# Kernel tuning notes

Hardware: AMD Instinct MI355X
Metric: run time of the kernel (lower is better)

## Reference

```python
import jax, jax.numpy as jnp
import numpy as np

B_, T, I, S, O = 64, 2048, 64, 128, 64

def setup_inputs() -> dict:
    key = jax.random.key(0)
    ks = jax.random.split(key, 7)
    x = jax.random.normal(ks[0], (B_, T, I), dtype=jnp.float32)
    A = jax.random.normal(ks[1], (S, S), dtype=jnp.float32) * 0.1
    Bm = jax.random.normal(ks[2], (S, I), dtype=jnp.float32) * 0.1
    Cm = jax.random.normal(ks[3], (O, S), dtype=jnp.float32) * 0.1
    Dm = jax.random.normal(ks[4], (O, I), dtype=jnp.float32) * 0.1
    W_sel = jax.random.normal(ks[5], (S, I), dtype=jnp.float32) * 0.1
    b_sel = jnp.zeros((S,), jnp.float32)
    ln_gamma = jnp.ones((S,), jnp.float32)
    ln_beta = jnp.zeros((S,), jnp.float32)
    conv_w = jax.random.normal(ks[6], (S, I, 3), dtype=jnp.float32) * 0.1  # Conv1d weight [out,in,k]
    conv_b = jnp.zeros((S,), jnp.float32)
    return {"x": x, "A": A, "B": Bm, "C": Cm, "D": Dm, "W_sel": W_sel,
            "b_sel": b_sel, "ln_gamma": ln_gamma, "ln_beta": ln_beta,
            "conv_w": conv_w, "conv_b": conv_b, "use_parallel": 0}

LN_EPS = 1e-5

def _forward(x, A, B, C, D, W_sel, b_sel, ln_gamma, ln_beta, conv_w, conv_b, use_parallel):
    # x: [B, T, I]
    if use_parallel and x.shape[1] > 10:
        # parallel_scan: conv1d(k=3, pad=1) -> cumsum over time -> project with C
        xc = jnp.transpose(x, (0, 2, 1))  # [B, I, T]
        conv = jax.lax.conv_general_dilated(
            xc, conv_w, window_strides=(1,), padding=((1, 1),),
            dimension_numbers=("NCH", "OIH", "NCH")) + conv_b[None, :, None]
        conv = jnp.transpose(conv, (0, 2, 1))           # [B, T, S]
        out = jnp.cumsum(conv, axis=1) @ C.T            # [B, T, O]
    else:
        # selective_scan: sequential gated SSM with per-step LayerNorm
        def step(h, x_t):
            gate = jax.nn.sigmoid(x_t @ W_sel.T + b_sel)        # [B, S]
            h_new = h @ A.T + x_t @ B.T
            h = gate * h_new + (1.0 - gate) * h
            mu = jnp.mean(h, axis=-1, keepdims=True)
            var = jnp.var(h, axis=-1, keepdims=True)
            h = (h - mu) * jax.lax.rsqrt(var + LN_EPS) * ln_gamma + ln_beta
            y = h @ C.T + x_t @ D.T                              # [B, O]
            return h, y
        h0 = jnp.zeros((x.shape[0], A.shape[0]), x.dtype)
        _, ys = jax.lax.scan(step, h0, jnp.transpose(x, (1, 0, 2)))  # ys: [T, B, O]
        out = jnp.transpose(ys, (1, 0, 2))                           # [B, T, O]
    final = out[:, -1, :]
    diff = jnp.diff(out, axis=1)
    temporal_coherence = 1.0 / (1.0 + jnp.mean(jnp.linalg.norm(diff, axis=-1)))
    state_magnitude = jnp.mean(jnp.linalg.norm(out, axis=-1))
    selection_activity = jnp.mean(jax.nn.sigmoid(jnp.mean(x, axis=1) @ W_sel.T + b_sel))
    state_stability = jnp.mean(jnp.std(out, axis=1, ddof=1))  # torch.std is unbiased
    return final, temporal_coherence, state_magnitude, selection_activity, state_stability

def reference(x, A, B, C, D, W_sel, b_sel, ln_gamma, ln_beta, conv_w, conv_b, use_parallel):
    return _forward(x, A, B, C, D, W_sel, b_sel, ln_gamma, ln_beta, conv_w, conv_b, use_parallel)
```

## Files before the change

### kernel.cpp

```cpp
#include <hip/hip_runtime.h>
#include <math.h>

#define NB 64
#define NT 2048
#define NI 64
#define NS 128
#define NO 64

typedef float4 f4;

#define PIN4(v) asm("" : "+v"((v).x), "+v"((v).y), "+v"((v).z), "+v"((v).w))

#define FMA4(a0,a1,a2,a3,W_,V_) \
    a0 = fmaf((W_).x, (V_).x, a0); a1 = fmaf((W_).y, (V_).y, a1); \
    a2 = fmaf((W_).z, (V_).z, a2); a3 = fmaf((W_).w, (V_).w, a3)

template<int CTRL>
__device__ __forceinline__ float dpp_add(float v) {
    int t = __builtin_amdgcn_update_dpp(0, __float_as_int(v), CTRL, 0xF, 0xF, true);
    return v + __int_as_float(t);
}
__device__ __forceinline__ float qxor1(float v) { return dpp_add<0xB1>(v); }
__device__ __forceinline__ float qxor2(float v) { return dpp_add<0x4E>(v); }
__device__ __forceinline__ float wave_sum63(float v) {
    v = dpp_add<0x111>(v); v = dpp_add<0x112>(v); v = dpp_add<0x114>(v);
    v = dpp_add<0x118>(v); v = dpp_add<0x142>(v); v = dpp_add<0x143>(v);
    return v;
}

__device__ __forceinline__ float sigmoidf_fast(float z) {
    float e = __builtin_amdgcn_exp2f(z * -1.442695041f);
    return __builtin_amdgcn_rcpf(1.0f + e);
}

__device__ __forceinline__ void bar_lds() {
    asm volatile("s_waitcnt lgkmcnt(0)" ::: "memory");
    __builtin_amdgcn_s_barrier();
    asm volatile("" ::: "memory");
}

__device__ __forceinline__ void stage16(const float* g, float* l) {
    __builtin_amdgcn_global_load_lds(
        (const __attribute__((address_space(1))) void*)g,
        (__attribute__((address_space(3))) void*)l, 16, 0, 0);
}

__global__ __launch_bounds__(512, 2) void scan_kernel(
    const float* __restrict__ x,
    const float* __restrict__ A,
    const float* __restrict__ Bm,
    const float* __restrict__ Wsel,
    const float* __restrict__ bsel,
    const float* __restrict__ gamma,
    const float* __restrict__ beta,
    float* __restrict__ H,
    float* __restrict__ musig)
{
    const int b    = blockIdx.x;
    const int tid  = threadIdx.x;
    const int q    = tid & 3;
    const int r    = tid >> 2;
    const int lane = tid & 63;
    const int wave = tid >> 6;

    __shared__ __align__(16) float hbuf[2][148];
    __shared__ __align__(16) float red[2][16];
    __shared__ __align__(16) float xlds[2][32][64];

    f4 Aw0, Aw1, Aw2, Aw3, Aw4, Aw5, Aw6, Aw7;
    float sAg = 0.f, aB = 0.f;
    {
        const f4* ga = (const f4*)(gamma + q * 32);
        const f4* bb = (const f4*)(beta  + q * 32);
        const f4* Ap = (const f4*)(A + (size_t)r * NS + q * 32);
        f4 g, be_, v;
#define LOADA(J, AW) \
        g = ga[J]; be_ = bb[J]; v = Ap[J]; \
        AW.x = v.x * g.x; AW.y = v.y * g.y; AW.z = v.z * g.z; AW.w = v.w * g.w; \
        sAg += (AW.x + AW.y) + (AW.z + AW.w); \
        aB = fmaf(v.x, be_.x, aB); aB = fmaf(v.y, be_.y, aB); \
        aB = fmaf(v.z, be_.z, aB); aB = fmaf(v.w, be_.w, aB);
        LOADA(0, Aw0) LOADA(1, Aw1) LOADA(2, Aw2) LOADA(3, Aw3)
        LOADA(4, Aw4) LOADA(5, Aw5) LOADA(6, Aw6) LOADA(7, Aw7)
#undef LOADA
        sAg = qxor2(qxor1(sAg));
        aB  = qxor2(qxor1(aB));
    }
    f4 Bw0, Bw1, Bw2, Bw3, Ww0, Ww1, Ww2, Ww3;
    {
        const f4* Bp = (const f4*)(Bm   + (size_t)r * NI + q * 16);
        const f4* Wp = (const f4*)(Wsel + (size_t)r * NI + q * 16);
        Bw0 = Bp[0]; Bw1 = Bp[1]; Bw2 = Bp[2]; Bw3 = Bp[3];
        Ww0 = Wp[0]; Ww1 = Wp[1]; Ww2 = Wp[2]; Ww3 = Wp[3];
    }
    float bs = bsel[r], gm = gamma[r], bt = beta[r];

    PIN4(Aw0); PIN4(Aw1); PIN4(Aw2); PIN4(Aw3);
    PIN4(Aw4); PIN4(Aw5); PIN4(Aw6); PIN4(Aw7);
    PIN4(Bw0); PIN4(Bw1); PIN4(Bw2); PIN4(Bw3);
    PIN4(Ww0); PIN4(Ww1); PIN4(Ww2); PIN4(Ww3);
    asm("" : "+v"(sAg), "+v"(aB), "+v"(bs), "+v"(gm), "+v"(bt));

    const float* xstage = x + (size_t)b * NT * NI + wave * 256 + lane * 4;
    stage16(xstage,        &xlds[0][wave * 4][0]);
    stage16(xstage + 2048, &xlds[1][wave * 4][0]);
    asm volatile("s_waitcnt vmcnt(0)" ::: "memory");
    __syncthreads();

    float zp, dBp;
    auto xdots = [&](int t) {
        const f4* xp = (const f4*)&xlds[(t >> 5) & 1][t & 31][q * 16];
        f4 v0 = xp[0], v1 = xp[1], v2 = xp[2], v3 = xp[3];
        float p0 = 0.f, p1 = 0.f, p2 = 0.f, p3 = 0.f;
        float w0 = 0.f, w1 = 0.f, w2 = 0.f, w3 = 0.f;
        FMA4(p0, p1, p2, p3, Bw0, v0); FMA4(p0, p1, p2, p3, Bw1, v1);
        FMA4(p0, p1, p2, p3, Bw2, v2); FMA4(p0, p1, p2, p3, Bw3, v3);
        FMA4(w0, w1, w2, w3, Ww0, v0); FMA4(w0, w1, w2, w3, Ww1, v1);
        FMA4(w0, w1, w2, w3, Ww2, v2); FMA4(w0, w1, w2, w3, Ww3, v3);
        dBp = qxor2(qxor1((p0 + p1) + (p2 + p3)));
        zp  = qxor2(qxor1((w0 + w1) + (w2 + w3))) + bs;
    };

    float*  Hb   = H + ((size_t)b * NT) * NS;
    float2* musb = (float2*)musig + (size_t)b * NT;

    float mp;
    xdots(0);
    {
        float g = sigmoidf_fast(zp);
        mp = g * dBp;
        if (q == 0) {
            hbuf[0][((r >> 5) * 36) + (r & 31)] = mp;
            Hb[r] = mp;
        }
        float s  = wave_sum63(mp);
        float s2 = wave_sum63(mp * mp);
        if (lane == 63) { red[0][wave] = s; red[0][8 + wave] = s2; }
    }
    xdots(1);
    bar_lds();

    auto body = [&](int t, int parIn, int parOut) {
        const f4* rp = (const f4*)&red[parIn][0];
        f4 sa = rp[0], sb = rp[1], sc = rp[2], sd = rp[3];
        float S  = ((sa.x + sa.y) + (sa.z + sa.w)) + ((sb.x + sb.y) + (sb.z + sb.w));
        float S2 = ((sc.x + sc.y) + (sc.z + sc.w)) + ((sd.x + sd.y) + (sd.z + sd.w));
        float mu   = S * (1.0f / 512.0f);
        float var  = fmaf(S2, 1.0f / 512.0f, -mu * mu);
        float rstd = 1.0f / sqrtf(var + 1e-5f);
        const f4* hp = (const f4*)&hbuf[parIn][q * 36];
        f4 h0 = hp[0], h1 = hp[1], h2 = hp[2], h3 = hp[3];
        f4 h4 = hp[4], h5 = hp[5], h6 = hp[6], h7 = hp[7];
        float d0 = 0.f, d1 = 0.f, d2 = 0.f, d3 = 0.f;
        FMA4(d0, d1, d2, d3, Aw0, h0); FMA4(d0, d1, d2, d3, Aw1, h1);
        FMA4(d0, d1, d2, d3, Aw2, h2); FMA4(d0, d1, d2, d3, Aw3, h3);
        FMA4(d0, d1, d2, d3, Aw4, h4); FMA4(d0, d1, d2, d3, Aw5, h5);
        FMA4(d0, d1, d2, d3, Aw6, h6); FMA4(d0, d1, d2, d3, Aw7, h7);
        float dAm = qxor2(qxor1((d0 + d1) + (d2 + d3)));
        float dA  = fmaf(rstd, fmaf(-mu, sAg, dAm), aB);
        float hpl = fmaf((mp - mu) * rstd, gm, bt);
        float g  = sigmoidf_fast(zp);
        float hn = dA + dBp;
        float m  = fmaf(g, hn - hpl, hpl);
        if (q == 0) {
            hbuf[parOut][((r >> 5) * 36) + (r & 31)] = m;
            Hb[(size_t)t * NS + r] = m;
        }
        float s  = wave_sum63(m);
        float s2 = wave_sum63(m * m);
        if (lane == 63) { red[parOut][wave] = s; red[parOut][8 + wave] = s2; }
        if (tid == 0) musb[t - 1] = make_float2(mu, rstd);
        mp = m;
        if (t + 1 < NT) xdots(t + 1);
        bar_lds();
    };

    auto boundary = [&](int t) {
        const int s2 = (t >> 5) + 2;
        if (s2 < NT / 32)
            stage16(xstage + (size_t)s2 * 2048, &xlds[s2 & 1][wave * 4][0]);
        asm volatile("s_waitcnt vmcnt(1)" ::: "memory");
        __builtin_amdgcn_s_barrier();
        asm volatile("" ::: "memory");
    };

    for (int t = 1; t + 1 < NT; t += 2) {
        body(t, 0, 1);
        body(t + 1, 1, 0);
        if (((t + 1) & 31) == 30) boundary(t + 1);
    }
    body(NT - 1, 0, 1);

    {
        const f4* rp = (const f4*)&red[1][0];
        f4 sa = rp[0], sb = rp[1], sc = rp[2], sd = rp[3];
        float S  = ((sa.x + sa.y) + (sa.z + sa.w)) + ((sb.x + sb.y) + (sb.z + sb.w));
        float S2 = ((sc.x + sc.y) + (sc.z + sc.w)) + ((sd.x + sd.y) + (sd.z + sd.w));
        float mu   = S * (1.0f / 512.0f);
        float var  = fmaf(S2, 1.0f / 512.0f, -mu * mu);
        float rstd = 1.0f / sqrtf(var + 1e-5f);
        if (tid == 0) musb[NT - 1] = make_float2(mu, rstd);
    }
}

#define CHUNKS 32
#define TCH (NT / CHUNKS)

__global__ __launch_bounds__(512, 2) void y_stats_kernel(
    const float* __restrict__ H,
    const float* __restrict__ x,
    const float* __restrict__ Cm,
    const float* __restrict__ Dm,
    const float* __restrict__ gamma,
    const float* __restrict__ beta,
    const float* __restrict__ musig,
    float* __restrict__ SY,
    float* __restrict__ SYY,
    float* __restrict__ meanx,
    float* __restrict__ nsum,
    float* __restrict__ dsum,
    float* __restrict__ outFinal)
{
    const int b     = blockIdx.x >> 5;
    const int chunk = blockIdx.x & 31;
    const int tid   = threadIdx.x;
    const int o     = tid & 63;
    const int sub   = tid >> 6;
    const int kh    = sub & 1;
    const int tg    = sub >> 1;
    const int lane  = tid & 63;

    __shared__ float pbuf[TCH + 1][2 * NO];
    __shared__ float nd[2];

    f4 C0,C1,C2,C3,C4,C5,C6,C7,C8,C9,C10,C11,C12,C13,C14,C15;
    float sCg = 0.f, cB = 0.f;
    {
        const f4* cp = (const f4*)(Cm + (size_t)o * NS + kh * 64);
        const f4* gp = (const f4*)(gamma + kh * 64);
        const f4* bp = (const f4*)(beta  + kh * 64);
        f4 v, g, be;
#define LOADC(J, CW) \
        v = cp[J]; g = gp[J]; be = bp[J]; \
        CW.x = v.x * g.x; CW.y = v.y * g.y; CW.z = v.z * g.z; CW.w = v.w * g.w; \
        sCg += (CW.x + CW.y) + (CW.z + CW.w); \
        cB = fmaf(v.x, be.x, cB); cB = fmaf(v.y, be.y, cB); \
        cB = fmaf(v.z, be.z, cB); cB = fmaf(v.w, be.w, cB);
        LOADC(0,C0) LOADC(1,C1) LOADC(2,C2) LOADC(3,C3)
        LOADC(4,C4) LOADC(5,C5) LOADC(6,C6) LOADC(7,C7)
        LOADC(8,C8) LOADC(9,C9) LOADC(10,C10) LOADC(11,C11)
        LOADC(12,C12) LOADC(13,C13) LOADC(14,C14) LOADC(15,C15)
#undef LOADC
    }
    f4 D0,D1,D2,D3,D4,D5,D6,D7;
    {
        const f4* dp = (const f4*)(Dm + (size_t)o * NI + kh * 32);
        D0 = dp[0]; D1 = dp[1]; D2 = dp[2]; D3 = dp[3];
        D4 = dp[4]; D5 = dp[5]; D6 = dp[6]; D7 = dp[7];
    }
    PIN4(C0); PIN4(C1); PIN4(C2); PIN4(C3); PIN4(C4); PIN4(C5); PIN4(C6); PIN4(C7);
    PIN4(C8); PIN4(C9); PIN4(C10); PIN4(C11); PIN4(C12); PIN4(C13); PIN4(C14); PIN4(C15);
    PIN4(D0); PIN4(D1); PIN4(D2); PIN4(D3); PIN4(D4); PIN4(D5); PIN4(D6); PIN4(D7);
    asm("" : "+v"(sCg), "+v"(cB));

    const float*  Hb  = H + ((size_t)b * NT) * NS;
    const float*  xb  = x + ((size_t)b * NT) * NI;
    const float2* msb = (const float2*)musig + (size_t)b * NT;
    const int t0 = chunk * TCH;

    if (tid < 2) nd[tid] = 0.f;

    if (sub < 4) {
        float s = 0.f;
        const float* xk = xb + o;
        #pragma unroll 4
        for (int i = 0; i < 16; ++i) s += xk[(size_t)(t0 + sub * 16 + i) * NI];
        atomicAdd(&meanx[b * NI + o], s);
    }

    {
        const int i_start = (tg == 0 && t0 > 0) ? -1 : 0;
        for (int i = i_start; i < 16; ++i) {
            const int t = t0 + tg * 16 + i;
            float2 ms = msb[t];
            const f4* hp = (const f4*)(Hb + (size_t)t * NS + kh * 64);
            const f4* xp = (const f4*)(xb + (size_t)t * NI + kh * 32);
            float y0 = 0.f, y1 = 0.f, y2 = 0.f, y3 = 0.f;
            f4 hv;
            hv = hp[0];  FMA4(y0,y1,y2,y3,C0,hv);
            hv = hp[1];  FMA4(y0,y1,y2,y3,C1,hv);
            hv = hp[2];  FMA4(y0,y1,y2,y3,C2,hv);
            hv = hp[3];  FMA4(y0,y1,y2,y3,C3,hv);
            hv = hp[4];  FMA4(y0,y1,y2,y3,C4,hv);
            hv = hp[5];  FMA4(y0,y1,y2,y3,C5,hv);
            hv = hp[6];  FMA4(y0,y1,y2,y3,C6,hv);
            hv = hp[7];  FMA4(y0,y1,y2,y3,C7,hv);
            hv = hp[8];  FMA4(y0,y1,y2,y3,C8,hv);
            hv = hp[9];  FMA4(y0,y1,y2,y3,C9,hv);
            hv = hp[10]; FMA4(y0,y1,y2,y3,C10,hv);
            hv = hp[11]; FMA4(y0,y1,y2,y3,C11,hv);
            hv = hp[12]; FMA4(y0,y1,y2,y3,C12,hv);
            hv = hp[13]; FMA4(y0,y1,y2,y3,C13,hv);
            hv = hp[14]; FMA4(y0,y1,y2,y3,C14,hv);
            hv = hp[15]; FMA4(y0,y1,y2,y3,C15,hv);
            float hdot = (y0 + y1) + (y2 + y3);
            float x0 = 0.f, x1 = 0.f, x2 = 0.f, x3 = 0.f;
            hv = xp[0];  FMA4(x0,x1,x2,x3,D0,hv);
            hv = xp[1];  FMA4(x0,x1,x2,x3,D1,hv);
            hv = xp[2];  FMA4(x0,x1,x2,x3,D2,hv);
            hv = xp[3];  FMA4(x0,x1,x2,x3,D3,hv);
            hv = xp[4];  FMA4(x0,x1,x2,x3,D4,hv);
            hv = xp[5];  FMA4(x0,x1,x2,x3,D5,hv);
            hv = xp[6];  FMA4(x0,x1,x2,x3,D6,hv);
            hv = xp[7];  FMA4(x0,x1,x2,x3,D7,hv);
            float xdot = (x0 + x1) + (x2 + x3);
            pbuf[tg * 16 + i + 1][kh * 64 + o] =
                fmaf(ms.y, fmaf(-ms.x, sCg, hdot), cB + xdot);
        }
    }
    __syncthreads();

    {
        const int tt0 = sub * 8;
        float yprev = pbuf[tt0][o] + pbuf[tt0][64 + o];
        float sy = 0.f, syy = 0.f, na = 0.f, da = 0.f;
        #pragma unroll
        for (int ii = 0; ii < 8; ++ii) {
            const int row = tt0 + ii + 1;
            float y = pbuf[row][o] + pbuf[row][64 + o];
            sy  += y;
            syy += y * y;
            float n2 = wave_sum63(y * y);
            na += sqrtf(n2);
            if (t0 + tt0 + ii > 0) {
                float df = y - yprev;
                float d2 = wave_sum63(df * df);
                da += sqrtf(d2);
            }
            yprev = y;
            if (chunk == 31 && sub == 7 && ii == 7)
                outFinal[b * NO + o] = y;
        }
        atomicAdd(&SY[b * NO + o], sy);
        atomicAdd(&SYY[b * NO + o], syy);
        if (lane == 63) {
            atomicAdd(&nd[0], na);
            atomicAdd(&nd[1], da);
        }
    }
    __syncthreads();
    if (tid == 0) { atomicAdd(nsum, nd[0]); atomicAdd(dsum, nd[1]); }
}

__global__ __launch_bounds__(256) void finalize_kernel(
    const float* __restrict__ Wsel,
    const float* __restrict__ bsel,
    const float* __restrict__ meanx,
    const float* __restrict__ SY,
    const float* __restrict__ SYY,
    const float* __restrict__ nsum,
    const float* __restrict__ dsum,
    float* __restrict__ out)
{
    const int tid  = threadIdx.x;
    const int wave = tid >> 6;
    const int lane = tid & 63;
    __shared__ float rs[8];

    float accsel = 0.f;
    for (int idx = tid; idx < NB * NS; idx += 256) {
        int bb = idx >> 7;
        int s  = idx & 127;
        const float* mp = meanx + bb * NI;
        const float* wp = Wsel  + (size_t)s * NI;
        float dot = 0.f;
        #pragma unroll 8
        for (int k = 0; k < NI; ++k) dot = fmaf(mp[k], wp[k], dot);
        float z = fmaf(dot, 1.0f / NT, bsel[s]);
        accsel += 1.0f / (1.0f + expf(-z));
    }
    float accss = 0.f;
    for (int idx = tid; idx < NB * NO; idx += 256) {
        float s1 = SY[idx], s2 = SYY[idx];
        float var = (s2 - s1 * s1 * (1.0f / NT)) * (1.0f / (NT - 1));
        accss += sqrtf(fmaxf(var, 0.0f));
    }
    #pragma unroll
    for (int d = 1; d < 64; d <<= 1) {
        accsel += __shfl_xor(accsel, d);
        accss  += __shfl_xor(accss, d);
    }
    if (lane == 0) { rs[wave] = accsel; rs[4 + wave] = accss; }
    __syncthreads();
    if (tid == 0) {
        float sel = (rs[0] + rs[1] + rs[2] + rs[3]) / (float)(NB * NS);
        float ss  = (rs[4] + rs[5] + rs[6] + rs[7]) / (float)(NB * NO);
        float tc  = 1.0f / (1.0f + dsum[0] / (float)(NB * (NT - 1)));
        float sm  = nsum[0] / (float)(NB * NT);
        out[4096] = tc;
        out[4097] = sm;
        out[4098] = sel;
        out[4099] = ss;
    }
}

extern "C" void kernel_launch(void* const* d_in, const int* in_sizes, int n_in,
                              void* d_out, int out_size, void* d_ws, size_t ws_size,
                              hipStream_t stream)
{
    (void)in_sizes; (void)n_in; (void)out_size; (void)ws_size;
    const float* x     = (const float*)d_in[0];
    const float* A     = (const float*)d_in[1];
    const float* Bm    = (const float*)d_in[2];
    const float* Cm    = (const float*)d_in[3];
    const float* Dm    = (const float*)d_in[4];
    const float* Wsel  = (const float*)d_in[5];
    const float* bsel  = (const float*)d_in[6];
    const float* gamma = (const float*)d_in[7];
    const float* beta  = (const float*)d_in[8];
    float* out = (float*)d_out;

    char* ws = (char*)d_ws;
    size_t off = 0;
    float* H     = (float*)(ws + off); off += (size_t)NB * NT * NS * sizeof(float);
    float* musig = (float*)(ws + off); off += (size_t)NB * NT * 2 * sizeof(float);
    char*  zbase = ws + off;
    float* SY    = (float*)(ws + off); off += NB * NO * sizeof(float);
    float* SYY   = (float*)(ws + off); off += NB * NO * sizeof(float);
    float* meanx = (float*)(ws + off); off += NB * NI * sizeof(float);
    float* nsum  = (float*)(ws + off); off += sizeof(float);
    float* dsum  = (float*)(ws + off); off += sizeof(float);
    size_t zbytes = (size_t)((char*)(dsum + 1) - zbase);

    hipMemsetAsync(zbase, 0, zbytes, stream);
    scan_kernel<<<NB, 512, 0, stream>>>(x, A, Bm, Wsel, bsel, gamma, beta, H, musig);
    y_stats_kernel<<<NB * CHUNKS, 512, 0, stream>>>(H, x, Cm, Dm, gamma, beta, musig,
                                                    SY, SYY, meanx, nsum, dsum, out);
    finalize_kernel<<<1, 256, 0, stream>>>(Wsel, bsel, meanx, SY, SYY, nsum, dsum, out);
}
```

Measured before the change: 1.943 ms.

## Precompute input projections in a parallel kernel before the sequential scan

Adds a parallel projection kernel that computes x·Bᵀ and x·W_selᵀ+b for all timesteps into a workspace buffer. The sequential scan then only reads the precomputed values from LDS, which takes those dot products and their cross-lane reductions off the serial critical path. The y_stats kernel is also reworked so each thread computes two output columns over a quarter of the state, combined with a lane shuffle. The cost is an extra 128 MB write/read of the projection buffer, a larger LDS staging footprint in the scan, and a fallback path when the workspace is too small.

```diff
diff --git a/kernel.cpp b/kernel.cpp
--- a/kernel.cpp
+++ b/kernel.cpp
@@ -10,7 +10,6 @@
 typedef float4 f4;
 
 #define PIN4(v) asm("" : "+v"((v).x), "+v"((v).y), "+v"((v).z), "+v"((v).w))
-
 #define FMA4(a0,a1,a2,a3,W_,V_) \
     a0 = fmaf((W_).x, (V_).x, a0); a1 = fmaf((W_).y, (V_).y, a1); \
     a2 = fmaf((W_).z, (V_).z, a2); a3 = fmaf((W_).w, (V_).w, a3)
@@ -27,26 +26,84 @@
     v = dpp_add<0x118>(v); v = dpp_add<0x142>(v); v = dpp_add<0x143>(v);
     return v;
 }
-
 __device__ __forceinline__ float sigmoidf_fast(float z) {
     float e = __builtin_amdgcn_exp2f(z * -1.442695041f);
     return __builtin_amdgcn_rcpf(1.0f + e);
 }
-
 __device__ __forceinline__ void bar_lds() {
     asm volatile("s_waitcnt lgkmcnt(0)" ::: "memory");
     __builtin_amdgcn_s_barrier();
     asm volatile("" ::: "memory");
 }
-
 __device__ __forceinline__ void stage16(const float* g, float* l) {
     __builtin_amdgcn_global_load_lds(
         (const __attribute__((address_space(1))) void*)g,
         (__attribute__((address_space(3))) void*)l, 16, 0, 0);
 }
 
+__global__ __launch_bounds__(256, 2) void proj_kernel(
+    const float* __restrict__ x,
+    const float* __restrict__ Bm,
+    const float* __restrict__ Wsel,
+    const float* __restrict__ bsel,
+    float* __restrict__ P)
+{
+    const int b   = blockIdx.x >> 5;
+    const int c   = blockIdx.x & 31;
+    const int tid = threadIdx.x;
+
+    __shared__ __align__(16) float xs[64][64];
+    {
+        const f4* src = (const f4*)(x + ((size_t)b * NT + c * 64) * NI);
+        f4* dst = (f4*)&xs[0][0];
+        #pragma unroll
+        for (int k = 0; k < 4; ++k) dst[tid + k * 256] = src[tid + k * 256];
+    }
+
+    const float* wrow = (tid < 128) ? (Bm + (size_t)tid * NI)
+                                    : (Wsel + (size_t)(tid - 128) * NI);
+    const float bias = (tid < 128) ? 0.f : bsel[tid - 128];
+
+    f4 W0,W1,W2,W3,W4,W5,W6,W7,W8,W9,W10,W11,W12,W13,W14,W15;
+    {
+        const f4* wp = (const f4*)wrow;
+        W0=wp[0]; W1=wp[1]; W2=wp[2]; W3=wp[3]; W4=wp[4]; W5=wp[5]; W6=wp[6]; W7=wp[7];
+        W8=wp[8]; W9=wp[9]; W10=wp[10]; W11=wp[11]; W12=wp[12]; W13=wp[13]; W14=wp[14]; W15=wp[15];
+    }
+    PIN4(W0); PIN4(W1); PIN4(W2); PIN4(W3); PIN4(W4); PIN4(W5); PIN4(W6); PIN4(W7);
+    PIN4(W8); PIN4(W9); PIN4(W10); PIN4(W11); PIN4(W12); PIN4(W13); PIN4(W14); PIN4(W15);
+
+    __syncthreads();
+
+    float* pout = P + ((size_t)b * NT + c * 64) * 256 + tid;
+    for (int t = 0; t < 64; ++t) {
+        const f4* xr = (const f4*)&xs[t][0];
+        float a0 = bias, a1 = 0.f, a2 = 0.f, a3 = 0.f;
+        f4 v;
+        v = xr[0];  FMA4(a0,a1,a2,a3,W0,v);
+        v = xr[1];  FMA4(a0,a1,a2,a3,W1,v);
+        v = xr[2];  FMA4(a0,a1,a2,a3,W2,v);
+        v = xr[3];  FMA4(a0,a1,a2,a3,W3,v);
+        v = xr[4];  FMA4(a0,a1,a2,a3,W4,v);
+        v = xr[5];  FMA4(a0,a1,a2,a3,W5,v);
+        v = xr[6];  FMA4(a0,a1,a2,a3,W6,v);
+        v = xr[7];  FMA4(a0,a1,a2,a3,W7,v);
+        v = xr[8];  FMA4(a0,a1,a2,a3,W8,v);
+        v = xr[9];  FMA4(a0,a1,a2,a3,W9,v);
+        v = xr[10]; FMA4(a0,a1,a2,a3,W10,v);
+        v = xr[11]; FMA4(a0,a1,a2,a3,W11,v);
+        v = xr[12]; FMA4(a0,a1,a2,a3,W12,v);
+        v = xr[13]; FMA4(a0,a1,a2,a3,W13,v);
+        v = xr[14]; FMA4(a0,a1,a2,a3,W14,v);
+        v = xr[15]; FMA4(a0,a1,a2,a3,W15,v);
+        pout[(size_t)t * 256] = (a0 + a1) + (a2 + a3);
+    }
+}
+
+template<int USEP>
 __global__ __launch_bounds__(512, 2) void scan_kernel(
     const float* __restrict__ x,
+    const float* __restrict__ P,
     const float* __restrict__ A,
     const float* __restrict__ Bm,
     const float* __restrict__ Wsel,
@@ -65,7 +122,7 @@
 
     __shared__ __align__(16) float hbuf[2][148];
     __shared__ __align__(16) float red[2][16];
-    __shared__ __align__(16) float xlds[2][32][64];
+    __shared__ __align__(16) float plds[2][32][USEP ? 256 : 64];
 
     f4 Aw0, Aw1, Aw2, Aw3, Aw4, Aw5, Aw6, Aw7;
     float sAg = 0.f, aB = 0.f;
@@ -86,30 +143,44 @@
         sAg = qxor2(qxor1(sAg));
         aB  = qxor2(qxor1(aB));
     }
+    PIN4(Aw0); PIN4(Aw1); PIN4(Aw2); PIN4(Aw3);
+    PIN4(Aw4); PIN4(Aw5); PIN4(Aw6); PIN4(Aw7);
+
     f4 Bw0, Bw1, Bw2, Bw3, Ww0, Ww1, Ww2, Ww3;
-    {
+    float bs = 0.f;
+    if constexpr (!USEP) {
         const f4* Bp = (const f4*)(Bm   + (size_t)r * NI + q * 16);
         const f4* Wp = (const f4*)(Wsel + (size_t)r * NI + q * 16);
         Bw0 = Bp[0]; Bw1 = Bp[1]; Bw2 = Bp[2]; Bw3 = Bp[3];
         Ww0 = Wp[0]; Ww1 = Wp[1]; Ww2 = Wp[2]; Ww3 = Wp[3];
-    }
-    float bs = bsel[r], gm = gamma[r], bt = beta[r];
-
-    PIN4(Aw0); PIN4(Aw1); PIN4(Aw2); PIN4(Aw3);
-    PIN4(Aw4); PIN4(Aw5); PIN4(Aw6); PIN4(Aw7);
-    PIN4(Bw0); PIN4(Bw1); PIN4(Bw2); PIN4(Bw3);
-    PIN4(Ww0); PIN4(Ww1); PIN4(Ww2); PIN4(Ww3);
-    asm("" : "+v"(sAg), "+v"(aB), "+v"(bs), "+v"(gm), "+v"(bt));
+        bs = bsel[r];
+        PIN4(Bw0); PIN4(Bw1); PIN4(Bw2); PIN4(Bw3);
+        PIN4(Ww0); PIN4(Ww1); PIN4(Ww2); PIN4(Ww3);
+        asm("" : "+v"(bs));
+    }
+    float gm = gamma[r], bt = beta[r];
+    asm("" : "+v"(sAg), "+v"(aB), "+v"(gm), "+v"(bt));
 
     const float* xstage = x + (size_t)b * NT * NI + wave * 256 + lane * 4;
-    stage16(xstage,        &xlds[0][wave * 4][0]);
-    stage16(xstage + 2048, &xlds[1][wave * 4][0]);
+    const float* pstage = P + (size_t)b * NT * 256 + wave * 256 + lane * 4;
+    if constexpr (USEP) {
+        #pragma unroll
+        for (int c = 0; c < 2; ++c)
+            #pragma unroll
+            for (int k = 0; k < 4; ++k)
+                stage16(pstage + (size_t)(c * 32 + k * 8) * 256,
+                        &plds[c][k * 8 + wave][0]);
+    } else {
+        stage16(xstage,        &plds[0][wave * 4][0]);
+        stage16(xstage + 2048, &plds[1][wave * 4][0]);
+    }
     asm volatile("s_waitcnt vmcnt(0)" ::: "memory");
     __syncthreads();
 
-    float zp, dBp;
+    float zp = 0.f, dBp = 0.f;
+    float pbp = 0.f, pzp = 0.f;
     auto xdots = [&](int t) {
-        const f4* xp = (const f4*)&xlds[(t >> 5) & 1][t & 31][q * 16];
+        const f4* xp = (const f4*)&plds[(t >> 5) & 1][t & 31][q * 16];
         f4 v0 = xp[0], v1 = xp[1], v2 = xp[2], v3 = xp[3];
         float p0 = 0.f, p1 = 0.f, p2 = 0.f, p3 = 0.f;
         float w0 = 0.f, w1 = 0.f, w2 = 0.f, w3 = 0.f;
@@ -120,15 +191,19 @@
         dBp = qxor2(qxor1((p0 + p1) + (p2 + p3)));
         zp  = qxor2(qxor1((w0 + w1) + (w2 + w3))) + bs;
     };
+    auto pread = [&](int t) {
+        const float* pl = &plds[(t >> 5) & 1][t & 31][0];
+        pbp = pl[r]; pzp = pl[128 + r];
+    };
 
     float*  Hb   = H + ((size_t)b * NT) * NS;
     float2* musb = (float2*)musig + (size_t)b * NT;
 
     float mp;
-    xdots(0);
-    {
-        float g = sigmoidf_fast(zp);
-        mp = g * dBp;
+    if constexpr (USEP) pread(0); else xdots(0);
+    {
+        float g = sigmoidf_fast(USEP ? pzp : zp);
+        mp = g * (USEP ? pbp : dBp);
         if (q == 0) {
             hbuf[0][((r >> 5) * 36) + (r & 31)] = mp;
             Hb[r] = mp;
@@ -137,7 +212,7 @@
         float s2 = wave_sum63(mp * mp);
         if (lane == 63) { red[0][wave] = s; red[0][8 + wave] = s2; }
     }
-    xdots(1);
+    if constexpr (USEP) pread(1); else xdots(1);
     bar_lds();
 
     auto body = [&](int t, int parIn, int parOut) {
@@ -159,9 +234,9 @@
         float dAm = qxor2(qxor1((d0 + d1) + (d2 + d3)));
         float dA  = fmaf(rstd, fmaf(-mu, sAg, dAm), aB);
         float hpl = fmaf((mp - mu) * rstd, gm, bt);
-        float g  = sigmoidf_fast(zp);
-        float hn = dA + dBp;
-        float m  = fmaf(g, hn - hpl, hpl);
+        float g   = sigmoidf_fast(USEP ? pzp : zp);
+        float hn  = dA + (USEP ? pbp : dBp);
+        float m   = fmaf(g, hn - hpl, hpl);
         if (q == 0) {
             hbuf[parOut][((r >> 5) * 36) + (r & 31)] = m;
             Hb[(size_t)t * NS + r] = m;
@@ -171,15 +246,25 @@
         if (lane == 63) { red[parOut][wave] = s; red[parOut][8 + wave] = s2; }
         if (tid == 0) musb[t - 1] = make_float2(mu, rstd);
         mp = m;
-        if (t + 1 < NT) xdots(t + 1);
+        if (t + 1 < NT) { if constexpr (USEP) pread(t + 1); else xdots(t + 1); }
         bar_lds();
     };
 
     auto boundary = [&](int t) {
         const int s2 = (t >> 5) + 2;
-        if (s2 < NT / 32)
-            stage16(xstage + (size_t)s2 * 2048, &xlds[s2 & 1][wave * 4][0]);
-        asm volatile("s_waitcnt vmcnt(1)" ::: "memory");
+        if constexpr (USEP) {
+            if (s2 < NT / 32) {
+                #pragma unroll
+                for (int k = 0; k < 4; ++k)
+                    stage16(pstage + (size_t)(s2 * 32 + k * 8) * 256,
+                            &plds[s2 & 1][k * 8 + wave][0]);
+            }
+            asm volatile("s_waitcnt vmcnt(4)" ::: "memory");
+        } else {
+            if (s2 < NT / 32)
+                stage16(xstage + (size_t)s2 * 2048, &plds[s2 & 1][wave * 4][0]);
+            asm volatile("s_waitcnt vmcnt(1)" ::: "memory");
+        }
         __builtin_amdgcn_s_barrier();
         asm volatile("" ::: "memory");
     };
@@ -206,7 +291,7 @@
 #define CHUNKS 32
 #define TCH (NT / CHUNKS)
 
-__global__ __launch_bounds__(512, 2) void y_stats_kernel(
+__global__ __launch_bounds__(512, 1) void y_stats_kernel(
     const float* __restrict__ H,
     const float* __restrict__ x,
     const float* __restrict__ Cm,
@@ -224,44 +309,47 @@
     const int b     = blockIdx.x >> 5;
     const int chunk = blockIdx.x & 31;
     const int tid   = threadIdx.x;
+    const int o2    = tid & 31;
+    const int kq    = (tid >> 5) & 3;
+    const int tg    = tid >> 7;
+    const int lane  = tid & 63;
+    const int sub   = tid >> 6;
     const int o     = tid & 63;
-    const int sub   = tid >> 6;
-    const int kh    = sub & 1;
-    const int tg    = sub >> 1;
-    const int lane  = tid & 63;
 
     __shared__ float pbuf[TCH + 1][2 * NO];
     __shared__ float nd[2];
 
-    f4 C0,C1,C2,C3,C4,C5,C6,C7,C8,C9,C10,C11,C12,C13,C14,C15;
-    float sCg = 0.f, cB = 0.f;
-    {
-        const f4* cp = (const f4*)(Cm + (size_t)o * NS + kh * 64);
-        const f4* gp = (const f4*)(gamma + kh * 64);
-        const f4* bp = (const f4*)(beta  + kh * 64);
-        f4 v, g, be;
-#define LOADC(J, CW) \
-        v = cp[J]; g = gp[J]; be = bp[J]; \
-        CW.x = v.x * g.x; CW.y = v.y * g.y; CW.z = v.z * g.z; CW.w = v.w * g.w; \
-        sCg += (CW.x + CW.y) + (CW.z + CW.w); \
-        cB = fmaf(v.x, be.x, cB); cB = fmaf(v.y, be.y, cB); \
-        cB = fmaf(v.z, be.z, cB); cB = fmaf(v.w, be.w, cB);
-        LOADC(0,C0) LOADC(1,C1) LOADC(2,C2) LOADC(3,C3)
-        LOADC(4,C4) LOADC(5,C5) LOADC(6,C6) LOADC(7,C7)
-        LOADC(8,C8) LOADC(9,C9) LOADC(10,C10) LOADC(11,C11)
-        LOADC(12,C12) LOADC(13,C13) LOADC(14,C14) LOADC(15,C15)
-#undef LOADC
-    }
-    f4 D0,D1,D2,D3,D4,D5,D6,D7;
-    {
-        const f4* dp = (const f4*)(Dm + (size_t)o * NI + kh * 32);
-        D0 = dp[0]; D1 = dp[1]; D2 = dp[2]; D3 = dp[3];
-        D4 = dp[4]; D5 = dp[5]; D6 = dp[6]; D7 = dp[7];
-    }
-    PIN4(C0); PIN4(C1); PIN4(C2); PIN4(C3); PIN4(C4); PIN4(C5); PIN4(C6); PIN4(C7);
-    PIN4(C8); PIN4(C9); PIN4(C10); PIN4(C11); PIN4(C12); PIN4(C13); PIN4(C14); PIN4(C15);
-    PIN4(D0); PIN4(D1); PIN4(D2); PIN4(D3); PIN4(D4); PIN4(D5); PIN4(D6); PIN4(D7);
-    asm("" : "+v"(sCg), "+v"(cB));
+    f4 CA0,CA1,CA2,CA3,CA4,CA5,CA6,CA7, CB0,CB1,CB2,CB3,CB4,CB5,CB6,CB7;
+    float sCgA = 0.f, cBA = 0.f, sCgB = 0.f, cBB = 0.f;
+    {
+        const f4* cpA = (const f4*)(Cm + (size_t)o2 * NS + kq * 32);
+        const f4* cpB = (const f4*)(Cm + (size_t)(o2 + 32) * NS + kq * 32);
+        const f4* gp  = (const f4*)(gamma + kq * 32);
+        const f4* bp  = (const f4*)(beta  + kq * 32);
+        f4 vv, gg, bb;
+#define LC(J, CW, CP, SG, CBs) \
+        vv = CP[J]; gg = gp[J]; bb = bp[J]; \
+        CW.x = vv.x * gg.x; CW.y = vv.y * gg.y; CW.z = vv.z * gg.z; CW.w = vv.w * gg.w; \
+        SG += (CW.x + CW.y) + (CW.z + CW.w); \
+        CBs = fmaf(vv.x, bb.x, CBs); CBs = fmaf(vv.y, bb.y, CBs); \
+        CBs = fmaf(vv.z, bb.z, CBs); CBs = fmaf(vv.w, bb.w, CBs);
+        LC(0,CA0,cpA,sCgA,cBA) LC(1,CA1,cpA,sCgA,cBA) LC(2,CA2,cpA,sCgA,cBA) LC(3,CA3,cpA,sCgA,cBA)
+        LC(4,CA4,cpA,sCgA,cBA) LC(5,CA5,cpA,sCgA,cBA) LC(6,CA6,cpA,sCgA,cBA) LC(7,CA7,cpA,sCgA,cBA)
+        LC(0,CB0,cpB,sCgB,cBB) LC(1,CB1,cpB,sCgB,cBB) LC(2,CB2,cpB,sCgB,cBB) LC(3,CB3,cpB,sCgB,cBB)
+        LC(4,CB4,cpB,sCgB,cBB) LC(5,CB5,cpB,sCgB,cBB) LC(6,CB6,cpB,sCgB,cBB) LC(7,CB7,cpB,sCgB,cBB)
+#undef LC
+    }
+    f4 DA0,DA1,DA2,DA3, DB0,DB1,DB2,DB3;
+    {
+        const f4* dpA = (const f4*)(Dm + (size_t)o2 * NI + kq * 16);
+        const f4* dpB = (const f4*)(Dm + (size_t)(o2 + 32) * NI + kq * 16);
+        DA0 = dpA[0]; DA1 = dpA[1]; DA2 = dpA[2]; DA3 = dpA[3];
+        DB0 = dpB[0]; DB1 = dpB[1]; DB2 = dpB[2]; DB3 = dpB[3];
+    }
+    PIN4(CA0); PIN4(CA1); PIN4(CA2); PIN4(CA3); PIN4(CA4); PIN4(CA5); PIN4(CA6); PIN4(CA7);
+    PIN4(CB0); PIN4(CB1); PIN4(CB2); PIN4(CB3); PIN4(CB4); PIN4(CB5); PIN4(CB6); PIN4(CB7);
+    PIN4(DA0); PIN4(DA1); PIN4(DA2); PIN4(DA3); PIN4(DB0); PIN4(DB1); PIN4(DB2); PIN4(DB3);
+    asm("" : "+v"(sCgA), "+v"(cBA), "+v"(sCgB), "+v"(cBB));
 
     const float*  Hb  = H + ((size_t)b * NT) * NS;
     const float*  xb  = x + ((size_t)b * NT) * NI;
@@ -279,43 +367,39 @@
     }
 
     {
+        const int khigh = sub & 1;
         const int i_start = (tg == 0 && t0 > 0) ? -1 : 0;
         for (int i = i_start; i < 16; ++i) {
             const int t = t0 + tg * 16 + i;
             float2 ms = msb[t];
-            const f4* hp = (const f4*)(Hb + (size_t)t * NS + kh * 64);
-            const f4* xp = (const f4*)(xb + (size_t)t * NI + kh * 32);
-            float y0 = 0.f, y1 = 0.f, y2 = 0.f, y3 = 0.f;
+            const f4* hp = (const f4*)(Hb + (size_t)t * NS + kq * 32);
+            const f4* xp = (const f4*)(xb + (size_t)t * NI + kq * 16);
+            float a0=0.f,a1=0.f,a2=0.f,a3=0.f, b0=0.f,b1=0.f,b2=0.f,b3=0.f;
             f4 hv;
-            hv = hp[0];  FMA4(y0,y1,y2,y3,C0,hv);
-            hv = hp[1];  FMA4(y0,y1,y2,y3,C1,hv);
-            hv = hp[2];  FMA4(y0,y1,y2,y3,C2,hv);
-            hv = hp[3];  FMA4(y0,y1,y2,y3,C3,hv);
-            hv = hp[4];  FMA4(y0,y1,y2,y3,C4,hv);
-            hv = hp[5];  FMA4(y0,y1,y2,y3,C5,hv);
-            hv = hp[6];  FMA4(y0,y1,y2,y3,C6,hv);
-            hv = hp[7];  FMA4(y0,y1,y2,y3,C7,hv);
-            hv = hp[8];  FMA4(y0,y1,y2,y3,C8,hv);
-            hv = hp[9];  FMA4(y0,y1,y2,y3,C9,hv);
-            hv = hp[10]; FMA4(y0,y1,y2,y3,C10,hv);
-            hv = hp[11]; FMA4(y0,y1,y2,y3,C11,hv);
-            hv = hp[12]; FMA4(y0,y1,y2,y3,C12,hv);
-            hv = hp[13]; FMA4(y0,y1,y2,y3,C13,hv);
-            hv = hp[14]; FMA4(y0,y1,y2,y3,C14,hv);
-            hv = hp[15]; FMA4(y0,y1,y2,y3,C15,hv);
-            float hdot = (y0 + y1) + (y2 + y3);
-            float x0 = 0.f, x1 = 0.f, x2 = 0.f, x3 = 0.f;
-            hv = xp[0];  FMA4(x0,x1,x2,x3,D0,hv);
-            hv = xp[1];  FMA4(x0,x1,x2,x3,D1,hv);
-            hv = xp[2];  FMA4(x0,x1,x2,x3,D2,hv);
-            hv = xp[3];  FMA4(x0,x1,x2,x3,D3,hv);
-            hv = xp[4];  FMA4(x0,x1,x2,x3,D4,hv);
-            hv = xp[5];  FMA4(x0,x1,x2,x3,D5,hv);
-            hv = xp[6];  FMA4(x0,x1,x2,x3,D6,hv);
-            hv = xp[7];  FMA4(x0,x1,x2,x3,D7,hv);
-            float xdot = (x0 + x1) + (x2 + x3);
-            pbuf[tg * 16 + i + 1][kh * 64 + o] =
-                fmaf(ms.y, fmaf(-ms.x, sCg, hdot), cB + xdot);
+            hv = hp[0]; FMA4(a0,a1,a2,a3,CA0,hv); FMA4(b0,b1,b2,b3,CB0,hv);
+            hv = hp[1]; FMA4(a0,a1,a2,a3,CA1,hv); FMA4(b0,b1,b2,b3,CB1,hv);
+            hv = hp[2]; FMA4(a0,a1,a2,a3,CA2,hv); FMA4(b0,b1,b2,b3,CB2,hv);
+            hv = hp[3]; FMA4(a0,a1,a2,a3,CA3,hv); FMA4(b0,b1,b2,b3,CB3,hv);
+            hv = hp[4]; FMA4(a0,a1,a2,a3,CA4,hv); FMA4(b0,b1,b2,b3,CB4,hv);
+            hv = hp[5]; FMA4(a0,a1,a2,a3,CA5,hv); FMA4(b0,b1,b2,b3,CB5,hv);
+            hv = hp[6]; FMA4(a0,a1,a2,a3,CA6,hv); FMA4(b0,b1,b2,b3,CB6,hv);
+            hv = hp[7]; FMA4(a0,a1,a2,a3,CA7,hv); FMA4(b0,b1,b2,b3,CB7,hv);
+            float hdotA = (a0 + a1) + (a2 + a3);
+            float hdotB = (b0 + b1) + (b2 + b3);
+            float xa0=0.f,xa1=0.f,xa2=0.f,xa3=0.f, xb0=0.f,xb1=0.f,xb2=0.f,xb3=0.f;
+            hv = xp[0]; FMA4(xa0,xa1,xa2,xa3,DA0,hv); FMA4(xb0,xb1,xb2,xb3,DB0,hv);
+            hv = xp[1]; FMA4(xa0,xa1,xa2,xa3,DA1,hv); FMA4(xb0,xb1,xb2,xb3,DB1,hv);
+            hv = xp[2]; FMA4(xa0,xa1,xa2,xa3,DA2,hv); FMA4(xb0,xb1,xb2,xb3,DB2,hv);
+            hv = xp[3]; FMA4(xa0,xa1,xa2,xa3,DA3,hv); FMA4(xb0,xb1,xb2,xb3,DB3,hv);
+            float xdotA = (xa0 + xa1) + (xa2 + xa3);
+            float xdotB = (xb0 + xb1) + (xb2 + xb3);
+            float pa = fmaf(ms.y, fmaf(-ms.x, sCgA, hdotA), cBA + xdotA);
+            float pb = fmaf(ms.y, fmaf(-ms.x, sCgB, hdotB), cBB + xdotB);
+            pa += __shfl_xor(pa, 32);
+            pb += __shfl_xor(pb, 32);
+            const int row = tg * 16 + i + 1;
+            const int col = khigh * 64 + o2 + ((lane >= 32) ? 32 : 0);
+            pbuf[row][col] = (lane >= 32) ? pb : pa;
         }
     }
     __syncthreads();
@@ -408,7 +492,7 @@
                               void* d_out, int out_size, void* d_ws, size_t ws_size,
                               hipStream_t stream)
 {
-    (void)in_sizes; (void)n_in; (void)out_size; (void)ws_size;
+    (void)in_sizes; (void)n_in; (void)out_size;
     const float* x     = (const float*)d_in[0];
     const float* A     = (const float*)d_in[1];
     const float* Bm    = (const float*)d_in[2];
@@ -421,19 +505,32 @@
     float* out = (float*)d_out;
 
     char* ws = (char*)d_ws;
-    size_t off = 0;
-    float* H     = (float*)(ws + off); off += (size_t)NB * NT * NS * sizeof(float);
-    float* musig = (float*)(ws + off); off += (size_t)NB * NT * 2 * sizeof(float);
-    char*  zbase = ws + off;
-    float* SY    = (float*)(ws + off); off += NB * NO * sizeof(float);
-    float* SYY   = (float*)(ws + off); off += NB * NO * sizeof(float);
-    float* meanx = (float*)(ws + off); off += NB * NI * sizeof(float);
-    float* nsum  = (float*)(ws + off); off += sizeof(float);
-    float* dsum  = (float*)(ws + off); off += sizeof(float);
-    size_t zbytes = (size_t)((char*)(dsum + 1) - zbase);
-
-    hipMemsetAsync(zbase, 0, zbytes, stream);
-    scan_kernel<<<NB, 512, 0, stream>>>(x, A, Bm, Wsel, bsel, gamma, beta, H, musig);
+    float* SY    = (float*)(ws + 0);
+    float* SYY   = (float*)(ws + 16384);
+    float* meanx = (float*)(ws + 32768);
+    float* nsum  = (float*)(ws + 49152);
+    float* dsum  = (float*)(ws + 49156);
+    const size_t zbytes = 49160;
+
+    const size_t offH  = 65536;
+    float* H     = (float*)(ws + offH);
+    const size_t offMu = offH + (size_t)NB * NT * NS * sizeof(float);
+    float* musig = (float*)(ws + offMu);
+    const size_t offP  = offMu + (size_t)NB * NT * 2 * sizeof(float);
+    float* P     = (float*)(ws + offP);
+    const size_t needP = offP + (size_t)NB * NT * 256 * sizeof(float);
+
+    const bool useP = (ws_size >= needP);
+
+    hipMemsetAsync(ws, 0, zbytes, stream);
+    if (useP) {
+        proj_kernel<<<NB * 32, 256, 0, stream>>>(x, Bm, Wsel, bsel, P);
+        scan_kernel<1><<<NB, 512, 0, stream>>>(x, P, A, Bm, Wsel, bsel,
+                                               gamma, beta, H, musig);
+    } else {
+        scan_kernel<0><<<NB, 512, 0, stream>>>(x, (const float*)ws, A, Bm, Wsel,
+                                               bsel, gamma, beta, H, musig);
+    }
     y_stats_kernel<<<NB * CHUNKS, 512, 0, stream>>>(H, x, Cm, Dm, gamma, beta, musig,
                                                     SY, SYY, meanx, nsum, dsum, out);
     finalize_kernel<<<1, 256, 0, stream>>>(Wsel, bsel, meanx, SY, SYY, nsum, dsum, out);
```

New measurement: 1.681 ms. 13.5% less time.
